# Performance work log

Measured on AMD Instinct MI355X. Metric: run time of the kernel, lower is better.

Reference implementation:

```python
import jax, jax.numpy as jnp
import numpy as np

N_CELLS_PER_SIDE = 16
MAX_K = 32
N_HEADS = 8
CHUNK = 128

_NEIGHBOR_OFFSETS = jnp.array([[-1, -1], [-1, 0], [-1, 1], [0, -1], [0, 0], [0, 1], [1, -1], [1, 0], [1, 1]], dtype=jnp.int32)


def cell_lookup(query_pos, cell_map, pos_min, pos_range):
    B, S, _ = query_pos.shape
    mpc = cell_map.shape[1]
    normalized = (query_pos - pos_min) / pos_range
    cell_xy = jnp.clip((normalized * N_CELLS_PER_SIDE).astype(jnp.int32), 0, N_CELLS_PER_SIDE - 1)
    nb = jnp.clip(cell_xy[:, :, None, :] + _NEIGHBOR_OFFSETS[None, None, :, :], 0, N_CELLS_PER_SIDE - 1)
    nidx = nb[..., 0] * N_CELLS_PER_SIDE + nb[..., 1]
    cand = cell_map[nidx].reshape(B, S, 9 * mpc)
    valid = cand >= 0
    return jnp.where(valid, cand, 0), valid


def threshold_gate(scores, tau, max_k):
    raw = scores - tau
    gate = jnp.where(raw > 0, raw, 1e-8 * jnp.exp(raw))
    eg = jnp.exp(gate) - 1.0
    k = min(max_k, scores.shape[-1])
    tv, _ = jax.lax.top_k(eg, k)
    eg = jnp.where(eg >= tv[:, :, -1:], eg, 0.0)
    gs = eg.sum(axis=-1, keepdims=True) + 1e-8
    strength = jnp.tanh(eg.max(axis=-1, keepdims=True))
    return eg / gs * strength


def setup_inputs() -> dict:
    key = jax.random.key(0)
    ks = jax.random.split(key, 16)
    B, S, D, N, P = 2, 1024, 512, 4096, 2
    n_cells, mpc = N_CELLS_PER_SIDE ** 2, 32
    return {
        "x": jax.random.normal(ks[0], (B, S, D), jnp.float32),
        "qk_pos": jax.random.uniform(ks[1], (B, S, P), jnp.float32),
        "v_pos": jax.random.uniform(ks[2], (B, S, P), jnp.float32),
        "tau_Q": jax.random.uniform(ks[3], (B, S, 1), jnp.float32),
        "tau_K": jax.random.uniform(ks[4], (B, S, 1), jnp.float32),
        "tau_V": jax.random.uniform(ks[5], (B, S, 1), jnp.float32),
        "qk_neurons": jax.random.normal(ks[6], (N, D), jnp.float32) / np.float32(np.sqrt(D)),
        "v_neurons": jax.random.normal(ks[7], (N, D), jnp.float32) / np.float32(np.sqrt(D)),
        "npos_qk": jax.random.uniform(ks[8], (N, P), jnp.float32),
        "npos_v": jax.random.uniform(ks[9], (N, P), jnp.float32),
        "cell_map_qk": jax.random.randint(ks[10], (n_cells, mpc), 0, N, jnp.int32),
        "cell_map_v": jax.random.randint(ks[11], (n_cells, mpc), 0, N, jnp.int32),
        "pos_min": jnp.zeros((P,), jnp.float32),
        "pos_range": jnp.ones((P,), jnp.float32),
        "expand_O": jax.random.normal(ks[12], (D, D), jnp.float32) * 0.02,
    }


def reference(x, qk_pos, v_pos, tau_Q, tau_K, tau_V, qk_neurons, v_neurons, npos_qk, npos_v, cell_map_qk, cell_map_v, pos_min, pos_range, expand_O):
    B, S, D = x.shape
    # full-sequence spatial cell lookup (small int tensors)
    ci_qk, m_qk = cell_lookup(qk_pos, cell_map_qk, pos_min, pos_range)
    ci_v, m_v = cell_lookup(v_pos, cell_map_v, pos_min, pos_range)
    ci_qk = jax.lax.stop_gradient(ci_qk)
    ci_v = jax.lax.stop_gradient(ci_v)
    nc = S // CHUNK  # S chosen divisible by CHUNK (no padding path needed)

    def chunks(a):
        return a.reshape(B, nc, CHUNK, *a.shape[2:]).swapaxes(0, 1)

    inp = tuple(map(chunks, (x, qk_pos, v_pos, tau_Q, tau_K, tau_V, ci_qk, m_qk, ci_v, m_v)))

    def step(carry, c):
        x_c, qkp, vp, tq, tk, tv, i_qk, mk, i_v, mv = c
        cand_qk = qk_neurons[i_qk]  # [B,C,n_cand,D]
        cand_v = v_neurons[i_v]
        act_qk = jnp.einsum('bsd,bsnd->bsn', x_c, cand_qk)
        act_v = jnp.einsum('bsd,bsnd->bsn', x_c, cand_v)
        s_qk = jnp.where(mk, act_qk, -1e9)
        s_v = jnp.where(mv, act_v, -1e9)
        gQ = threshold_gate(s_qk, tq, MAX_K)
        gK = threshold_gate(s_qk, tk, MAX_K)
        gV = threshold_gate(s_v, tv, MAX_K)
        Q_c = jnp.einsum('bsn,bsnd->bsd', act_qk * gQ * mk, cand_qk)
        K_c = jnp.einsum('bsn,bsnd->bsd', act_qk * gK * mk, cand_qk)
        V_c = jnp.einsum('bsn,bsnd->bsd', act_v * gV * mv, cand_v)
        pd_qk = jnp.sum((qkp[:, :, None, :] - npos_qk[i_qk]) ** 2, axis=-1)
        pl_qk = (jax.lax.stop_gradient(gQ) * pd_qk * mk).sum() / (mk.sum() + 1e-8)
        pd_v = jnp.sum((vp[:, :, None, :] - npos_v[i_v]) ** 2, axis=-1)
        pl_v = (jax.lax.stop_gradient(gV) * pd_v * mv).sum() / (mv.sum() + 1e-8)
        return carry, (Q_c, K_c, V_c, pl_qk + pl_v)

    _, (Qs, Ks, Vs, pls) = jax.lax.scan(step, 0, inp)

    def merge(a):
        return a.swapaxes(0, 1).reshape(B, S, D)

    Q, K, V = merge(Qs), merge(Ks), merge(Vs)
    pos_loss = pls.mean()  # == sum / n_chunks

    dh = D // N_HEADS
    Qh = Q.reshape(B, S, N_HEADS, dh).transpose(0, 2, 1, 3)
    Kh = K.reshape(B, S, N_HEADS, dh).transpose(0, 2, 1, 3)
    Vh = V.reshape(B, S, N_HEADS, dh).transpose(0, 2, 1, 3)
    scores = jnp.einsum('bhsd,bhtd->bhst', Qh, Kh) / jnp.sqrt(jnp.float32(dh))
    causal = jnp.tril(jnp.ones((S, S), dtype=jnp.bool_))
    scores = jnp.where(causal, scores, jnp.finfo(scores.dtype).min)
    attn = jax.nn.softmax(scores, axis=-1)
    out = jnp.einsum('bhst,bhtd->bhsd', attn, Vh)
    out = out.transpose(0, 2, 1, 3).reshape(B, S, D)
    out = out @ expand_O
    return out, pos_loss
```

## Files before the change

kernel.cpp:

```cpp
#include <hip/hip_runtime.h>
#include <math.h>

#define B_ 2
#define S_ 1024
#define D_ 512
#define N_ 4096
#define H_ 8
#define DH_ 64
#define NCAND 288
#define TOPK 32
#define NTOK (B_*S_)
#define NG2 1152

#define NROWS 16384
#define NSLOT_BH 8704
#define NSLOTS (16*NSLOT_BH)

typedef __attribute__((ext_vector_type(8))) short short8;
typedef __attribute__((ext_vector_type(4))) float f32x4;

__device__ __forceinline__ float wave_sum(float v) {
    #pragma unroll
    for (int o = 32; o; o >>= 1) v += __shfl_xor(v, o);
    return v;
}
__device__ __forceinline__ float wave_max(float v) {
    #pragma unroll
    for (int o = 32; o; o >>= 1) v = fmaxf(v, __shfl_xor(v, o));
    return v;
}
__device__ __forceinline__ ushort f2b_rn(float f) {
    unsigned u = __float_as_uint(f);
    return (ushort)((u + 0x7FFFu + ((u >> 16) & 1u)) >> 16);
}
__device__ __forceinline__ float b2f(ushort h) {
    return __uint_as_float(((unsigned)h) << 16);
}
__device__ __forceinline__ int swzi(int row, int c8) {
    return row * 64 + ((c8 ^ (row & 7)) << 3);
}

__global__ __launch_bounds__(1024) void sort_tokens_kernel(
    const float* __restrict__ qk_pos, const float* __restrict__ v_pos,
    const float* __restrict__ pos_min, const float* __restrict__ pos_range,
    int* __restrict__ order_qk, int* __restrict__ order_v,
    int2* __restrict__ desc_qk, int2* __restrict__ desc_v,
    float* __restrict__ posacc)
{
    __shared__ int hist[256], tmp[256], offs[256], startc[256], gcnt[256];
    const int t = threadIdx.x;
    const int pass = blockIdx.x;
    if (pass == 0 && t < 32) posacc[t] = 0.f;
    const float pm0 = pos_min[0], pm1 = pos_min[1];
    const float pr0 = pos_range[0], pr1 = pos_range[1];
    const float* pos = pass ? v_pos : qk_pos;
    int* order = pass ? order_v : order_qk;
    int2* desc = pass ? desc_v : desc_qk;
    if (t < NG2) desc[t] = make_int2(0, 0);
    if (t + 1024 < NG2) desc[t + 1024] = make_int2(0, 0);
    if (t < 256) hist[t] = 0;
    __syncthreads();
    int cell[2];
    #pragma unroll
    for (int k = 0; k < 2; k++) {
        int tok = t + k * 1024;
        float p0 = pos[tok * 2], p1 = pos[tok * 2 + 1];
        int cx = min(max((int)((p0 - pm0) / pr0 * 16.f), 0), 15);
        int cy = min(max((int)((p1 - pm1) / pr1 * 16.f), 0), 15);
        cell[k] = cx * 16 + cy;
        atomicAdd(&hist[cell[k]], 1);
    }
    __syncthreads();
    if (t < 256) tmp[t] = hist[t];
    __syncthreads();
    for (int d = 1; d < 256; d <<= 1) {
        int v = 0;
        if (t < 256 && t >= d) v = tmp[t - d];
        __syncthreads();
        if (t < 256) tmp[t] += v;
        __syncthreads();
    }
    if (t < 256) {
        startc[t] = tmp[t] - hist[t];
        offs[t]   = startc[t];
        gcnt[t]   = (hist[t] + 1) >> 1;
    }
    __syncthreads();
    #pragma unroll
    for (int k = 0; k < 2; k++) {
        int tok = t + k * 1024;
        int p = atomicAdd(&offs[cell[k]], 1);
        order[p] = tok;
    }
    __syncthreads();
    if (t < 256) tmp[t] = gcnt[t];
    __syncthreads();
    for (int d = 1; d < 256; d <<= 1) {
        int v = 0;
        if (t < 256 && t >= d) v = tmp[t - d];
        __syncthreads();
        if (t < 256) tmp[t] += v;
        __syncthreads();
    }
    if (t < 256) {
        int g0 = tmp[t] - gcnt[t];
        for (int k = 0; k < gcnt[t]; k++)
            desc[g0 + k] = make_int2(startc[t] + 2 * k, min(2, hist[t] - 2 * k));
    }
}

__global__ __launch_bounds__(256) void qkv_fused(
    const int2* __restrict__ desc_qk, const int* __restrict__ order_qk,
    const int2* __restrict__ desc_v,  const int* __restrict__ order_v,
    const float* __restrict__ x,
    const float* __restrict__ qk_pos, const float* __restrict__ v_pos,
    const float* __restrict__ tauQ, const float* __restrict__ tauK,
    const float* __restrict__ tauV,
    const float* __restrict__ qk_neurons, const float* __restrict__ v_neurons,
    const float* __restrict__ npos_qk, const float* __restrict__ npos_v,
    const int* __restrict__ cm_qk, const int* __restrict__ cm_v,
    const float* __restrict__ pos_min, const float* __restrict__ pos_range,
    float* __restrict__ Q, float* __restrict__ K, float* __restrict__ V,
    float* __restrict__ posacc)
{
    const int bid = blockIdx.x;
    const int role = bid & 1;
    const int g = bid >> 1;
    const int gid = (g & 7) * 144 + (g >> 3);
    const int2 dsc = role ? desc_v[gid] : desc_qk[gid];
    const int gstart = dsc.x, count = dsc.y;
    if (count == 0) return;

    const int*   order   = role ? order_v   : order_qk;
    const float* pose    = role ? v_pos     : qk_pos;
    const float* neurons = role ? v_neurons : qk_neurons;
    const float* npos    = role ? npos_v    : npos_qk;
    const int*   cmap    = role ? cm_v      : cm_qk;

    __shared__ int   idx[NCAND];
    __shared__ float msk[NCAND];
    __shared__ float act[2][NCAND];
    __shared__ int   ci[2][NCAND];
    __shared__ float cw1[2][NCAND], cw2[2][NCAND];
    __shared__ int   toks[2], cnt2[2];
    __shared__ float red[2][2][4];
    __shared__ float redc;

    const int t = threadIdx.x, wid = t >> 6, lane = t & 63;
    const int sub = lane & 15, grp = lane >> 4;
    if (t < 2) { toks[t] = order[gstart + min(t, count - 1)]; cnt2[t] = 0; }
    __syncthreads();
    const int token0 = toks[0];

    const float pm0 = pos_min[0], pm1 = pos_min[1];
    const float pr0 = pos_range[0], pr1 = pos_range[1];
    {
        const float p0 = pose[token0 * 2], p1 = pose[token0 * 2 + 1];
        const int cx = min(max((int)((p0 - pm0) / pr0 * 16.f), 0), 15);
        const int cy = min(max((int)((p1 - pm1) / pr1 * 16.f), 0), 15);
        for (int c = t; c < NCAND; c += 256) {
            int o = c >> 5, ms = c & 31;
            int nx = min(max(cx + o / 3 - 1, 0), 15), ny = min(max(cy + o % 3 - 1, 0), 15);
            int cand = cmap[(nx * 16 + ny) * 32 + ms];
            idx[c] = cand >= 0 ? cand : 0;
            msk[c] = cand >= 0 ? 1.f : 0.f;
        }
    }
    __syncthreads();

    float4 xr0[8], xr1[8];
    {
        const float4* xp0 = (const float4*)(x + (size_t)toks[0] * D_);
        const float4* xp1 = (const float4*)(x + (size_t)toks[1] * D_);
        #pragma unroll
        for (int k = 0; k < 8; k++) {
            xr0[k] = xp0[k * 16 + sub];
            xr1[k] = xp1[k * 16 + sub];
        }
    }

    const int cb = wid * 72;
    for (int u = 0; u < 72; u += 4) {
        const int c = cb + u + grp;
        const float4* rp = (const float4*)(neurons + (size_t)idx[c] * D_);
        float a0 = 0.f, a1 = 0.f, b0 = 0.f, b1 = 0.f;
        #pragma unroll
        for (int k = 0; k < 8; k += 2) {
            float4 r0 = rp[k * 16 + sub];
            float4 r1 = rp[(k + 1) * 16 + sub];
            a0 += xr0[k].x*r0.x + xr0[k].y*r0.y + xr0[k].z*r0.z + xr0[k].w*r0.w;
            a1 += xr1[k].x*r0.x + xr1[k].y*r0.y + xr1[k].z*r0.z + xr1[k].w*r0.w;
            b0 += xr0[k+1].x*r1.x + xr0[k+1].y*r1.y + xr0[k+1].z*r1.z + xr0[k+1].w*r1.w;
            b1 += xr1[k+1].x*r1.x + xr1[k+1].y*r1.y + xr1[k+1].z*r1.z + xr1[k+1].w*r1.w;
        }
        float f0 = a0 + b0, f1 = a1 + b1;
        #pragma unroll
        for (int o = 1; o <= 8; o <<= 1) {
            f0 += __shfl_xor(f0, o);
            f1 += __shfl_xor(f1, o);
        }
        if (sub == 0) {
            const float mv = msk[c];
            act[0][c] = (mv != 0.f) ? f0 : -1e9f;
            act[1][c] = (mv != 0.f) ? f1 : -1e9f;
        }
    }
    __syncthreads();

    const int tk = wid >> 1, sw = wid & 1, tt = t & 127;
    const int token = toks[tk];

    if (sw == 0) {
        unsigned ej[5];
        #pragma unroll
        for (int k = 0; k < 5; k++) {
            int j = lane + 64 * k;
            float f = (j < NCAND) ? act[tk][j] : -1e30f;
            unsigned uu = __float_as_uint(f);
            ej[k] = (uu & 0x80000000u) ? ~uu : (uu | 0x80000000u);
        }
        unsigned T = 0u;
        for (int bit = 31; bit >= 0; bit--) {
            const unsigned cand = T | (1u << bit);
            int c = 0;
            #pragma unroll
            for (int k = 0; k < 5; k++)
                c += __popcll(__ballot(ej[k] >= cand));
            if (c >= TOPK) T = cand;
        }
        int base = 0;
        const unsigned long long below = (lane == 0) ? 0ull
                                       : (~0ull >> (64 - lane));
        #pragma unroll
        for (int k = 0; k < 5; k++) {
            const unsigned long long mk2 = __ballot(ej[k] >= T);
            if (ej[k] >= T) {
                int pos = base + __popcll(mk2 & below);
                ci[tk][pos] = lane + 64 * k;
            }
            base += __popcll(mk2);
        }
        if (lane == 0) cnt2[tk] = base;
    }
    if (wid == 0) {
        float cmv = 0.f;
        for (int c = lane; c < NCAND; c += 64) cmv += msk[c];
        cmv = wave_sum(cmv);
        if (lane == 0) redc = cmv;
    }
    __syncthreads();
    const float cm = redc;
    const int n = cnt2[tk];

    if (role == 0) {
        const float tq = tauQ[token], tkk = tauK[token];
        float sQ = 0.f, sK = 0.f, mQ = 0.f, mK = 0.f;
        for (int p = tt; p < n; p += 128) {
            float s = act[tk][ci[tk][p]];
            float rq = s - tq;
            float gq = (rq > 0.f) ? rq : 1e-8f * __expf(rq);
            float egq = __expf(gq) - 1.f;
            float rk = s - tkk;
            float gk = (rk > 0.f) ? rk : 1e-8f * __expf(rk);
            float egk = __expf(gk) - 1.f;
            cw1[tk][p] = egq; cw2[tk][p] = egk;
            sQ += egq; sK += egk;
            mQ = fmaxf(mQ, egq); mK = fmaxf(mK, egk);
        }
        sQ = wave_sum(sQ); mQ = wave_max(mQ);
        sK = wave_sum(sK); mK = wave_max(mK);
        if (lane == 0) {
            red[tk][sw][0] = sQ; red[tk][sw][1] = mQ;
            red[tk][sw][2] = sK; red[tk][sw][3] = mK;
        }
        __syncthreads();
        const float scQ = tanhf(fmaxf(red[tk][0][1], red[tk][1][1]))
                        / (red[tk][0][0] + red[tk][1][0] + 1e-8f);
        const float scK = tanhf(fmaxf(red[tk][0][3], red[tk][1][3]))
                        / (red[tk][0][2] + red[tk][1][2] + 1e-8f);
        __syncthreads();

        const float qp0 = pose[token * 2], qp1 = pose[token * 2 + 1];
        float plq = 0.f;
        for (int p = tt; p < n; p += 128) {
            int e = ci[tk][p];
            int id = idx[e];
            float m = msk[e], a = act[tk][e];
            float gq = cw1[tk][p] * scQ;
            cw1[tk][p] = a * gq * m;
            cw2[tk][p] = a * cw2[tk][p] * scK * m;
            ci[tk][p] = id;
            float d0 = qp0 - npos[id * 2], d1 = qp1 - npos[id * 2 + 1];
            plq += gq * (d0 * d0 + d1 * d1) * m;
        }
        plq = wave_sum(plq);
        if (lane == 0) red[tk][sw][0] = plq;
        __syncthreads();
        if (tt == 0 && tk < count) {
            int chunk = (token & 1023) >> 7;
            atomicAdd(&posacc[chunk], red[tk][0][0] + red[tk][1][0]);
            atomicAdd(&posacc[8 + chunk], cm);
        }

        if (tk < count) {
            float4 qa = {0,0,0,0}, ka = {0,0,0,0};
            int p = 0;
            for (; p + 1 < n; p += 2) {
                const float4 rA = *(const float4*)(neurons + (size_t)ci[tk][p] * D_ + tt * 4);
                const float4 rB = *(const float4*)(neurons + (size_t)ci[tk][p + 1] * D_ + tt * 4);
                const float wA = cw1[tk][p], bA = cw2[tk][p];
                const float wB = cw1[tk][p + 1], bB = cw2[tk][p + 1];
                qa.x += wA * rA.x + wB * rB.x; qa.y += wA * rA.y + wB * rB.y;
                qa.z += wA * rA.z + wB * rB.z; qa.w += wA * rA.w + wB * rB.w;
                ka.x += bA * rA.x + bB * rB.x; ka.y += bA * rA.y + bB * rB.y;
                ka.z += bA * rA.z + bB * rB.z; ka.w += bA * rA.w + bB * rB.w;
            }
            if (p < n) {
                const float4 rA = *(const float4*)(neurons + (size_t)ci[tk][p] * D_ + tt * 4);
                const float wA = cw1[tk][p], bA = cw2[tk][p];
                qa.x += wA * rA.x; qa.y += wA * rA.y; qa.z += wA * rA.z; qa.w += wA * rA.w;
                ka.x += bA * rA.x; ka.y += bA * rA.y; ka.z += bA * rA.z; ka.w += bA * rA.w;
            }
            *(float4*)(Q + (size_t)token * D_ + tt * 4) = qa;
            *(float4*)(K + (size_t)token * D_ + tt * 4) = ka;
        }
    } else {
        const float tv = tauV[token];
        float sV = 0.f, mV = 0.f;
        for (int p = tt; p < n; p += 128) {
            float s = act[tk][ci[tk][p]];
            float rv = s - tv;
            float gv = (rv > 0.f) ? rv : 1e-8f * __expf(rv);
            float egv = __expf(gv) - 1.f;
            cw1[tk][p] = egv;
            sV += egv; mV = fmaxf(mV, egv);
        }
        sV = wave_sum(sV); mV = wave_max(mV);
        if (lane == 0) { red[tk][sw][0] = sV; red[tk][sw][1] = mV; }
        __syncthreads();
        const float scV = tanhf(fmaxf(red[tk][0][1], red[tk][1][1]))
                        / (red[tk][0][0] + red[tk][1][0] + 1e-8f);
        __syncthreads();

        const float vp0 = pose[token * 2], vp1 = pose[token * 2 + 1];
        float plv = 0.f;
        for (int p = tt; p < n; p += 128) {
            int e = ci[tk][p];
            int id = idx[e];
            float m = msk[e], a = act[tk][e];
            float gv = cw1[tk][p] * scV;
            cw1[tk][p] = a * gv * m;
            ci[tk][p] = id;
            float d0 = vp0 - npos[id * 2], d1 = vp1 - npos[id * 2 + 1];
            plv += gv * (d0 * d0 + d1 * d1) * m;
        }
        plv = wave_sum(plv);
        if (lane == 0) red[tk][sw][0] = plv;
        __syncthreads();
        if (tt == 0 && tk < count) {
            int chunk = (token & 1023) >> 7;
            atomicAdd(&posacc[16 + chunk], red[tk][0][0] + red[tk][1][0]);
            atomicAdd(&posacc[24 + chunk], cm);
        }

        if (tk < count) {
            float4 va = {0,0,0,0};
            int p = 0;
            for (; p + 1 < n; p += 2) {
                const float4 rA = *(const float4*)(neurons + (size_t)ci[tk][p] * D_ + tt * 4);
                const float4 rB = *(const float4*)(neurons + (size_t)ci[tk][p + 1] * D_ + tt * 4);
                const float wA = cw1[tk][p], wB = cw1[tk][p + 1];
                va.x += wA * rA.x + wB * rB.x; va.y += wA * rA.y + wB * rB.y;
                va.z += wA * rA.z + wB * rB.z; va.w += wA * rA.w + wB * rB.w;
            }
            if (p < n) {
                const float4 rA = *(const float4*)(neurons + (size_t)ci[tk][p] * D_ + tt * 4);
                const float wA = cw1[tk][p];
                va.x += wA * rA.x; va.y += wA * rA.y; va.z += wA * rA.z; va.w += wA * rA.w;
            }
            *(float4*)(V + (size_t)token * D_ + tt * 4) = va;
        }
    }
}

__global__ __launch_bounds__(256) void wprep_kernel(
    const float* __restrict__ W, ushort* __restrict__ Wth, ushort* __restrict__ Wtl)
{
    __shared__ float tile[64][65];
    const int bx = blockIdx.x & 7, by = blockIdx.x >> 3;
    const int t = threadIdx.x;
    const int r = t >> 4, c4 = (t & 15) * 4;
    #pragma unroll
    for (int rr = 0; rr < 64; rr += 16) {
        const float4 v = *(const float4*)(W + (size_t)(by * 64 + rr + r) * 512 + bx * 64 + c4);
        *(float4*)&tile[rr + r][c4] = v;
    }
    __syncthreads();
    #pragma unroll
    for (int cc = 0; cc < 64; cc += 16) {
        const int c = cc + r;
        ushort h[4], l[4];
        #pragma unroll
        for (int i = 0; i < 4; i++) {
            float f = tile[c4 + i][c];
            h[i] = f2b_rn(f);
            l[i] = f2b_rn(f - b2f(h[i]));
        }
        *(uint2*)&Wth[(size_t)(bx * 64 + c) * 512 + by * 64 + c4] = *(uint2*)h;
        *(uint2*)&Wtl[(size_t)(bx * 64 + c) * 512 + by * 64 + c4] = *(uint2*)l;
    }
}

__global__ __launch_bounds__(256, 2) void attn_partial_kernel(
    const float* __restrict__ Q, const float* __restrict__ K,
    const float* __restrict__ V,
    float* __restrict__ pm, float* __restrict__ pl, float* __restrict__ po)
{
    const int xx = blockIdx.x & 7;
    int kq = blockIdx.x >> 3;
    const int bh = xx + 8 * (kq >= 72);
    kq = (kq >= 72) ? kq - 72 : kq;
    int rblk = 0;
    while (kq >= 2 * (rblk + 1)) { kq -= 2 * (rblk + 1); rblk++; }
    const int sp = kq;
    const int b = bh >> 3, h = bh & 7;
    const int j0 = sp * 64;
    const int rbase = rblk * 128;

    __shared__ __align__(16) ushort sKhi[64 * 64], sKlo[64 * 64];
    __shared__ __align__(16) ushort sVthi[64 * 64], sVtlo[64 * 64];
    __shared__ __align__(16) float sPool[8192];

    const int t = threadIdx.x;
    const int w = t >> 6, lane = t & 63;
    const int g = lane >> 4, ln = lane & 15;

    {
        const int srow = t >> 2, scol = (t & 3) << 4;
        const float* Kg = K + ((size_t)(b * S_ + j0 + srow)) * D_ + h * DH_ + scol;
        const float* Vg = V + ((size_t)(b * S_ + j0 + srow)) * D_ + h * DH_ + scol;
        union { float4 f4[4]; float f[16]; } kf, vf;
        kf.f4[0] = *(const float4*)(Kg);
        kf.f4[1] = *(const float4*)(Kg + 4);
        kf.f4[2] = *(const float4*)(Kg + 8);
        kf.f4[3] = *(const float4*)(Kg + 12);
        vf.f4[0] = *(const float4*)(Vg);
        vf.f4[1] = *(const float4*)(Vg + 4);
        vf.f4[2] = *(const float4*)(Vg + 8);
        vf.f4[3] = *(const float4*)(Vg + 12);
        union { uint4 d[2]; ushort u[16]; } uh, ul;
        #pragma unroll
        for (int i = 0; i < 16; i++) {
            uh.u[i] = f2b_rn(kf.f[i]);
            ul.u[i] = f2b_rn(kf.f[i] - b2f(uh.u[i]));
        }
        const int c8 = (t & 3) << 1;
        *(uint4*)&sKhi[swzi(srow, c8)]     = uh.d[0];
        *(uint4*)&sKhi[swzi(srow, c8 + 1)] = uh.d[1];
        *(uint4*)&sKlo[swzi(srow, c8)]     = ul.d[0];
        *(uint4*)&sKlo[swzi(srow, c8 + 1)] = ul.d[1];
        #pragma unroll
        for (int i = 0; i < 16; i++) sPool[srow * 65 + scol + i] = vf.f[i];
    }
    __syncthreads();
    {
        const int drow = t >> 2, kcol = (t & 3) << 4;
        union { uint4 d[2]; ushort u[16]; } uh, ul;
        #pragma unroll
        for (int i = 0; i < 16; i++) {
            const float f = sPool[(kcol + i) * 65 + drow];
            uh.u[i] = f2b_rn(f);
            ul.u[i] = f2b_rn(f - b2f(uh.u[i]));
        }
        const int c8 = (t & 3) << 1;
        *(uint4*)&sVthi[swzi(drow, c8)]     = uh.d[0];
        *(uint4*)&sVthi[swzi(drow, c8 + 1)] = uh.d[1];
        *(uint4*)&sVtlo[swzi(drow, c8)]     = ul.d[0];
        *(uint4*)&sVtlo[swzi(drow, c8 + 1)] = ul.d[1];
    }
    __syncthreads();

    const int wrow = rbase + w * 32;
    if (wrow + 31 < j0) return;

    ushort* sPw = (ushort*)sPool + w * 4096;

    short8 qhi[2][2], qlo[2][2];
    #pragma unroll
    for (int qt = 0; qt < 2; qt++) {
        const int qrow = wrow + qt * 16 + ln;
        const float* Qg = Q + ((size_t)(b * S_ + qrow)) * D_ + h * DH_ + g * 8;
        #pragma unroll
        for (int ds = 0; ds < 2; ds++) {
            union { float4 f4[2]; float f[8]; } qf;
            qf.f4[0] = *(const float4*)(Qg + ds * 32);
            qf.f4[1] = *(const float4*)(Qg + ds * 32 + 4);
            union { short8 v; ushort u[8]; } uh, ul;
            #pragma unroll
            for (int i = 0; i < 8; i++) {
                uh.u[i] = f2b_rn(qf.f[i]);
                ul.u[i] = f2b_rn(qf.f[i] - b2f(uh.u[i]));
            }
            qhi[qt][ds] = uh.v; qlo[qt][ds] = ul.v;
        }
    }

    const f32x4 fzero = {0.f, 0.f, 0.f, 0.f};
    f32x4 sT[2][4];
    #pragma unroll
    for (int qt = 0; qt < 2; qt++)
        #pragma unroll
        for (int kt = 0; kt < 4; kt++)
            sT[qt][kt] = fzero;
    #pragma unroll
    for (int ds = 0; ds < 2; ds++) {
        #pragma unroll
        for (int kt = 0; kt < 4; kt++) {
            const int krow = kt * 16 + ln;
            const short8 khi = *(const short8*)&sKhi[swzi(krow, ds * 4 + g)];
            const short8 klo = *(const short8*)&sKlo[swzi(krow, ds * 4 + g)];
            #pragma unroll
            for (int qt = 0; qt < 2; qt++) {
                sT[qt][kt] = __builtin_amdgcn_mfma_f32_16x16x32_bf16(khi, qhi[qt][ds], sT[qt][kt], 0, 0, 0);
                sT[qt][kt] = __builtin_amdgcn_mfma_f32_16x16x32_bf16(khi, qlo[qt][ds], sT[qt][kt], 0, 0, 0);
                sT[qt][kt] = __builtin_amdgcn_mfma_f32_16x16x32_bf16(klo, qhi[qt][ds], sT[qt][kt], 0, 0, 0);
            }
        }
    }

    #pragma unroll
    for (int qt = 0; qt < 2; qt++) {
        const int qg = wrow + qt * 16 + ln;
        float pv[16];
        float mq = -1e30f;
        #pragma unroll
        for (int kt = 0; kt < 4; kt++)
            #pragma unroll
            for (int r = 0; r < 4; r++) {
                const int kg = j0 + kt * 16 + g * 4 + r;
                float s = sT[qt][kt][r] * 0.125f;
                s = (kg <= qg) ? s : -1e30f;
                pv[kt * 4 + r] = s;
                mq = fmaxf(mq, s);
            }
        mq = fmaxf(mq, __shfl_xor(mq, 16));
        mq = fmaxf(mq, __shfl_xor(mq, 32));
        const float base = (mq < -1e29f) ? 0.f : mq;
        float lq = 0.f;
        #pragma unroll
        for (int i = 0; i < 16; i++) {
            const float e = __expf(pv[i] - base);
            pv[i] = e;
            lq += e;
        }
        lq += __shfl_xor(lq, 16);
        lq += __shfl_xor(lq, 32);

        const int qrow = qt * 16 + ln;
        #pragma unroll
        for (int kt = 0; kt < 4; kt++) {
            union { uint2 d; ushort u[4]; } h4, l4;
            #pragma unroll
            for (int r = 0; r < 4; r++) {
                const float f = pv[kt * 4 + r];
                h4.u[r] = f2b_rn(f);
                l4.u[r] = f2b_rn(f - b2f(h4.u[r]));
            }
            const int c8 = kt * 2 + (g >> 1);
            const int idx = qrow * 64 + ((c8 ^ (qrow & 7)) << 3) + ((g & 1) << 2);
            *(uint2*)&sPw[idx] = h4.d;
            *(uint2*)&sPw[2048 + idx] = l4.d;
        }
        if (g == 0 && qg >= j0) {
            const int gr = qg >> 6;
            const size_t slot = (size_t)bh * NSLOT_BH + 32 * gr * (gr + 1)
                              + (size_t)(qg & 63) * (gr + 1) + sp;
            pm[slot] = mq; pl[slot] = lq;
        }
    }

    f32x4 ot[4][2];
    #pragma unroll
    for (int dt = 0; dt < 4; dt++)
        #pragma unroll
        for (int qt = 0; qt < 2; qt++)
            ot[dt][qt] = fzero;
    #pragma unroll
    for (int ks = 0; ks < 2; ks++) {
        short8 pfh[2], pfl[2];
        #pragma unroll
        for (int qt = 0; qt < 2; qt++) {
            const int qrow = qt * 16 + ln;
            const int idx = qrow * 64 + (((ks * 4 + g) ^ (qrow & 7)) << 3);
            pfh[qt] = *(const short8*)&sPw[idx];
            pfl[qt] = *(const short8*)&sPw[2048 + idx];
        }
        #pragma unroll
        for (int dt = 0; dt < 4; dt++) {
            const int drow = dt * 16 + ln;
            const short8 vh = *(const short8*)&sVthi[swzi(drow, ks * 4 + g)];
            const short8 vl = *(const short8*)&sVtlo[swzi(drow, ks * 4 + g)];
            #pragma unroll
            for (int qt = 0; qt < 2; qt++) {
                ot[dt][qt] = __builtin_amdgcn_mfma_f32_16x16x32_bf16(vh, pfh[qt], ot[dt][qt], 0, 0, 0);
                ot[dt][qt] = __builtin_amdgcn_mfma_f32_16x16x32_bf16(vh, pfl[qt], ot[dt][qt], 0, 0, 0);
                ot[dt][qt] = __builtin_amdgcn_mfma_f32_16x16x32_bf16(vl, pfh[qt], ot[dt][qt], 0, 0, 0);
            }
        }
    }

    #pragma unroll
    for (int qt = 0; qt < 2; qt++) {
        const int qg = wrow + qt * 16 + ln;
        if (qg < j0) continue;
        const int gr = qg >> 6;
        const size_t slot = (size_t)bh * NSLOT_BH + 32 * gr * (gr + 1)
                          + (size_t)(qg & 63) * (gr + 1) + sp;
        float* od = po + slot * 64 + g * 4;
        #pragma unroll
        for (int dt = 0; dt < 4; dt++)
            *(f32x4*)(od + dt * 16) = ot[dt][qt];
    }
}

__global__ __launch_bounds__(256) void attn_combine_kernel(
    const float* __restrict__ pm, const float* __restrict__ pl,
    const float* __restrict__ po, float* __restrict__ AO)
{
    const int gth = blockIdx.x * 256 + threadIdx.x;
    const int r = gth >> 6, d = gth & 63;
    const int i = r & 1023, bh = r >> 10;
    const int b = bh >> 3, h = bh & 7;
    const int g = i >> 6;
    const int ns = g + 1;
    const size_t slot0 = (size_t)bh * NSLOT_BH + 32 * g * (g + 1)
                       + (size_t)(i & 63) * (g + 1);
    float mstar = -INFINITY, lstar = 0.f, ostar = 0.f;
    for (int s = 0; s < ns; s++) {
        const float mi = pm[slot0 + s];
        const float nm = fmaxf(mstar, mi);
        const float a = __expf(mstar - nm);
        const float w = __expf(mi - nm);
        lstar = lstar * a + pl[slot0 + s] * w;
        ostar = ostar * a + po[(slot0 + s) * 64 + d] * w;
        mstar = nm;
    }
    AO[((size_t)(b * S_ + i)) * D_ + h * DH_ + d] = ostar / lstar;
}

__global__ __launch_bounds__(256) void proj_kernel(
    const float* __restrict__ A,
    const ushort* __restrict__ Wth, const ushort* __restrict__ Wtl,
    float* __restrict__ out)
{
    const int tb = (blockIdx.x >> 4) * 64;
    const int cb = (blockIdx.x & 15) * 32;
    const int t = threadIdx.x, w = t >> 6, lane = t & 63;
    const int ln = lane & 15, ko = (lane >> 4) * 8;
    const int tok = tb + w * 16 + ln;

    const f32x4 fz = {0.f, 0.f, 0.f, 0.f};
    f32x4 acc[2];
    acc[0] = fz; acc[1] = fz;

    const float* Ap = A + (size_t)tok * 512 + ko;
    #pragma unroll 4
    for (int ks = 0; ks < 512; ks += 32) {
        union { float4 f4[2]; float f[8]; } af;
        af.f4[0] = *(const float4*)(Ap + ks);
        af.f4[1] = *(const float4*)(Ap + ks + 4);
        union { short8 v; ushort u[8]; } ah, al;
        #pragma unroll
        for (int i = 0; i < 8; i++) {
            ah.u[i] = f2b_rn(af.f[i]);
            al.u[i] = f2b_rn(af.f[i] - b2f(ah.u[i]));
        }
        #pragma unroll
        for (int ct = 0; ct < 2; ct++) {
            const size_t wb = (size_t)(cb + ct * 16 + ln) * 512 + ks + ko;
            const short8 bh = *(const short8*)(Wth + wb);
            const short8 bl = *(const short8*)(Wtl + wb);
            acc[ct] = __builtin_amdgcn_mfma_f32_16x16x32_bf16(ah.v, bh, acc[ct], 0, 0, 0);
            acc[ct] = __builtin_amdgcn_mfma_f32_16x16x32_bf16(al.v, bh, acc[ct], 0, 0, 0);
            acc[ct] = __builtin_amdgcn_mfma_f32_16x16x32_bf16(ah.v, bl, acc[ct], 0, 0, 0);
        }
    }
    #pragma unroll
    for (int ct = 0; ct < 2; ct++) {
        #pragma unroll
        for (int r = 0; r < 4; r++) {
            const int row = tb + w * 16 + (lane >> 4) * 4 + r;
            out[(size_t)row * 512 + cb + ct * 16 + ln] = acc[ct][r];
        }
    }
}

__global__ void ploss_kernel(const float* __restrict__ acc, float* __restrict__ out) {
    float ssum = 0.f;
    for (int c = 0; c < 8; c++) {
        ssum += acc[c]      / (acc[8 + c]  + 1e-8f);
        ssum += acc[16 + c] / (acc[24 + c] + 1e-8f);
    }
    out[0] = ssum * 0.125f;
}

extern "C" void kernel_launch(void* const* d_in, const int* in_sizes, int n_in,
                              void* d_out, int out_size, void* d_ws, size_t ws_size,
                              hipStream_t stream) {
    const float* x          = (const float*)d_in[0];
    const float* qk_pos     = (const float*)d_in[1];
    const float* v_pos      = (const float*)d_in[2];
    const float* tauQ       = (const float*)d_in[3];
    const float* tauK       = (const float*)d_in[4];
    const float* tauV       = (const float*)d_in[5];
    const float* qk_neurons = (const float*)d_in[6];
    const float* v_neurons  = (const float*)d_in[7];
    const float* npos_qk    = (const float*)d_in[8];
    const float* npos_v     = (const float*)d_in[9];
    const int*   cm_qk      = (const int*)d_in[10];
    const int*   cm_v       = (const int*)d_in[11];
    const float* pos_min    = (const float*)d_in[12];
    const float* pos_range  = (const float*)d_in[13];
    const float* expand_O   = (const float*)d_in[14];

    float* ws = (float*)d_ws;
    const size_t TDf = (size_t)NTOK * D_;
    float* Q   = ws;
    float* K   = ws + TDf;
    float* V   = ws + 2 * TDf;
    float* AO  = ws + 3 * TDf;
    float* acc = ws + 4 * TDf;
    int*   order_qk = (int*)(ws + 4 * TDf + 64);
    int*   order_v  = order_qk + NTOK;
    int2*  desc_qk  = (int2*)(order_v + NTOK);
    int2*  desc_v   = desc_qk + NG2;
    const size_t head = 4 * TDf + 64 + 2 * NTOK + 4 * NG2;

    float* pm = ws + head;
    float* pl = pm + (size_t)NSLOTS;
    float* po = pl + (size_t)NSLOTS;
    ushort* Wth = (ushort*)(po + (size_t)NSLOTS * 64);
    ushort* Wtl = Wth + 512 * 512;

    float* out = (float*)d_out;

    sort_tokens_kernel<<<2, 1024, 0, stream>>>(qk_pos, v_pos, pos_min, pos_range,
                                               order_qk, order_v, desc_qk, desc_v,
                                               acc);
    wprep_kernel<<<64, 256, 0, stream>>>(expand_O, Wth, Wtl);
    qkv_fused<<<2 * NG2, 256, 0, stream>>>(desc_qk, order_qk, desc_v, order_v,
                                           x, qk_pos, v_pos, tauQ, tauK, tauV,
                                           qk_neurons, v_neurons, npos_qk, npos_v,
                                           cm_qk, cm_v, pos_min, pos_range,
                                           Q, K, V, acc);
    attn_partial_kernel<<<1152, 256, 0, stream>>>(Q, K, V, pm, pl, po);
    attn_combine_kernel<<<(NROWS * 64) / 256, 256, 0, stream>>>(pm, pl, po, AO);
    proj_kernel<<<512, 256, 0, stream>>>(AO, Wth, Wtl, out);
    ploss_kernel<<<1, 1, 0, stream>>>(acc, out + TDf);
}
```

Baseline: 256.0 us.

## Emit bf16 hi/lo Q and K from QKV kernel, read directly in attention

The QKV kernel now writes Q and K as split bf16 hi/lo pairs, so the attention kernel no longer repeats the fp32-to-bf16 split on every tile it loads. K is read straight from global memory into MFMA operands instead of going through shared memory, which drops the K LDS buffers and their staging. The single-thread ploss kernel is folded into the projection kernel to save a launch. The trade-off is that K loads are now scattered global reads served from cache rather than swizzled LDS reads. Q and K traffic stays the same size, since two 16-bit halves replace one 32-bit value.

```diff
diff --git a/kernel.cpp b/kernel.cpp
--- a/kernel.cpp
+++ b/kernel.cpp
@@ -120,7 +120,9 @@
     const float* __restrict__ npos_qk, const float* __restrict__ npos_v,
     const int* __restrict__ cm_qk, const int* __restrict__ cm_v,
     const float* __restrict__ pos_min, const float* __restrict__ pos_range,
-    float* __restrict__ Q, float* __restrict__ K, float* __restrict__ V,
+    ushort* __restrict__ Qh, ushort* __restrict__ Ql,
+    ushort* __restrict__ Kh, ushort* __restrict__ Kl,
+    float* __restrict__ V,
     float* __restrict__ posacc)
 {
     const int bid = blockIdx.x;
@@ -321,8 +323,19 @@
                 qa.x += wA * rA.x; qa.y += wA * rA.y; qa.z += wA * rA.z; qa.w += wA * rA.w;
                 ka.x += bA * rA.x; ka.y += bA * rA.y; ka.z += bA * rA.z; ka.w += bA * rA.w;
             }
-            *(float4*)(Q + (size_t)token * D_ + tt * 4) = qa;
-            *(float4*)(K + (size_t)token * D_ + tt * 4) = ka;
+            float qv[4] = {qa.x, qa.y, qa.z, qa.w};
+            float kv[4] = {ka.x, ka.y, ka.z, ka.w};
+            ushort qh4[4], ql4[4], kh4[4], kl4[4];
+            #pragma unroll
+            for (int i = 0; i < 4; i++) {
+                qh4[i] = f2b_rn(qv[i]); ql4[i] = f2b_rn(qv[i] - b2f(qh4[i]));
+                kh4[i] = f2b_rn(kv[i]); kl4[i] = f2b_rn(kv[i] - b2f(kh4[i]));
+            }
+            const size_t qo = (size_t)token * D_ + tt * 4;
+            *(uint2*)(Qh + qo) = *(uint2*)qh4;
+            *(uint2*)(Ql + qo) = *(uint2*)ql4;
+            *(uint2*)(Kh + qo) = *(uint2*)kh4;
+            *(uint2*)(Kl + qo) = *(uint2*)kl4;
         }
     } else {
         const float tv = tauV[token];
@@ -412,7 +425,8 @@
 }
 
 __global__ __launch_bounds__(256, 2) void attn_partial_kernel(
-    const float* __restrict__ Q, const float* __restrict__ K,
+    const ushort* __restrict__ Qh, const ushort* __restrict__ Ql,
+    const ushort* __restrict__ Kh, const ushort* __restrict__ Kl,
     const float* __restrict__ V,
     float* __restrict__ pm, float* __restrict__ pl, float* __restrict__ po)
 {
@@ -427,7 +441,6 @@
     const int j0 = sp * 64;
     const int rbase = rblk * 128;
 
-    __shared__ __align__(16) ushort sKhi[64 * 64], sKlo[64 * 64];
     __shared__ __align__(16) ushort sVthi[64 * 64], sVtlo[64 * 64];
     __shared__ __align__(16) float sPool[8192];
 
@@ -437,30 +450,15 @@
 
     {
         const int srow = t >> 2, scol = (t & 3) << 4;
-        const float* Kg = K + ((size_t)(b * S_ + j0 + srow)) * D_ + h * DH_ + scol;
         const float* Vg = V + ((size_t)(b * S_ + j0 + srow)) * D_ + h * DH_ + scol;
-        union { float4 f4[4]; float f[16]; } kf, vf;
-        kf.f4[0] = *(const float4*)(Kg);
-        kf.f4[1] = *(const float4*)(Kg + 4);
-        kf.f4[2] = *(const float4*)(Kg + 8);
-        kf.f4[3] = *(const float4*)(Kg + 12);
-        vf.f4[0] = *(const float4*)(Vg);
-        vf.f4[1] = *(const float4*)(Vg + 4);
-        vf.f4[2] = *(const float4*)(Vg + 8);
-        vf.f4[3] = *(const float4*)(Vg + 12);
-        union { uint4 d[2]; ushort u[16]; } uh, ul;
-        #pragma unroll
-        for (int i = 0; i < 16; i++) {
-            uh.u[i] = f2b_rn(kf.f[i]);
-            ul.u[i] = f2b_rn(kf.f[i] - b2f(uh.u[i]));
-        }
-        const int c8 = (t & 3) << 1;
-        *(uint4*)&sKhi[swzi(srow, c8)]     = uh.d[0];
-        *(uint4*)&sKhi[swzi(srow, c8 + 1)] = uh.d[1];
-        *(uint4*)&sKlo[swzi(srow, c8)]     = ul.d[0];
-        *(uint4*)&sKlo[swzi(srow, c8 + 1)] = ul.d[1];
-        #pragma unroll
-        for (int i = 0; i < 16; i++) sPool[srow * 65 + scol + i] = vf.f[i];
+        float4 v0 = *(const float4*)(Vg);
+        float4 v1 = *(const float4*)(Vg + 4);
+        float4 v2 = *(const float4*)(Vg + 8);
+        float4 v3 = *(const float4*)(Vg + 12);
+        *(float4*)&sPool[srow * 65 + scol]      = v0;
+        *(float4*)&sPool[srow * 65 + scol + 4]  = v1;
+        *(float4*)&sPool[srow * 65 + scol + 8]  = v2;
+        *(float4*)&sPool[srow * 65 + scol + 12] = v3;
     }
     __syncthreads();
     {
@@ -489,19 +487,11 @@
     #pragma unroll
     for (int qt = 0; qt < 2; qt++) {
         const int qrow = wrow + qt * 16 + ln;
-        const float* Qg = Q + ((size_t)(b * S_ + qrow)) * D_ + h * DH_ + g * 8;
+        const size_t qb = ((size_t)(b * S_ + qrow)) * D_ + h * DH_ + g * 8;
         #pragma unroll
         for (int ds = 0; ds < 2; ds++) {
-            union { float4 f4[2]; float f[8]; } qf;
-            qf.f4[0] = *(const float4*)(Qg + ds * 32);
-            qf.f4[1] = *(const float4*)(Qg + ds * 32 + 4);
-            union { short8 v; ushort u[8]; } uh, ul;
-            #pragma unroll
-            for (int i = 0; i < 8; i++) {
-                uh.u[i] = f2b_rn(qf.f[i]);
-                ul.u[i] = f2b_rn(qf.f[i] - b2f(uh.u[i]));
-            }
-            qhi[qt][ds] = uh.v; qlo[qt][ds] = ul.v;
+            qhi[qt][ds] = *(const short8*)(Qh + qb + ds * 32);
+            qlo[qt][ds] = *(const short8*)(Ql + qb + ds * 32);
         }
     }
 
@@ -517,8 +507,9 @@
         #pragma unroll
         for (int kt = 0; kt < 4; kt++) {
             const int krow = kt * 16 + ln;
-            const short8 khi = *(const short8*)&sKhi[swzi(krow, ds * 4 + g)];
-            const short8 klo = *(const short8*)&sKlo[swzi(krow, ds * 4 + g)];
+            const size_t kb = ((size_t)(b * S_ + j0 + krow)) * D_ + h * DH_ + ds * 32 + g * 8;
+            const short8 khi = *(const short8*)(Kh + kb);
+            const short8 klo = *(const short8*)(Kl + kb);
             #pragma unroll
             for (int qt = 0; qt < 2; qt++) {
                 sT[qt][kt] = __builtin_amdgcn_mfma_f32_16x16x32_bf16(khi, qhi[qt][ds], sT[qt][kt], 0, 0, 0);
@@ -651,8 +642,17 @@
 __global__ __launch_bounds__(256) void proj_kernel(
     const float* __restrict__ A,
     const ushort* __restrict__ Wth, const ushort* __restrict__ Wtl,
-    float* __restrict__ out)
+    const float* __restrict__ acc,
+    float* __restrict__ out, float* __restrict__ outp)
 {
+    if (blockIdx.x == 0 && threadIdx.x == 0) {
+        float ssum = 0.f;
+        for (int c = 0; c < 8; c++) {
+            ssum += acc[c]      / (acc[8 + c]  + 1e-8f);
+            ssum += acc[16 + c] / (acc[24 + c] + 1e-8f);
+        }
+        outp[0] = ssum * 0.125f;
+    }
     const int tb = (blockIdx.x >> 4) * 64;
     const int cb = (blockIdx.x & 15) * 32;
     const int t = threadIdx.x, w = t >> 6, lane = t & 63;
@@ -660,8 +660,8 @@
     const int tok = tb + w * 16 + ln;
 
     const f32x4 fz = {0.f, 0.f, 0.f, 0.f};
-    f32x4 acc[2];
-    acc[0] = fz; acc[1] = fz;
+    f32x4 acc2[2];
+    acc2[0] = fz; acc2[1] = fz;
 
     const float* Ap = A + (size_t)tok * 512 + ko;
     #pragma unroll 4
@@ -680,9 +680,9 @@
             const size_t wb = (size_t)(cb + ct * 16 + ln) * 512 + ks + ko;
             const short8 bh = *(const short8*)(Wth + wb);
             const short8 bl = *(const short8*)(Wtl + wb);
-            acc[ct] = __builtin_amdgcn_mfma_f32_16x16x32_bf16(ah.v, bh, acc[ct], 0, 0, 0);
-            acc[ct] = __builtin_amdgcn_mfma_f32_16x16x32_bf16(al.v, bh, acc[ct], 0, 0, 0);
-            acc[ct] = __builtin_amdgcn_mfma_f32_16x16x32_bf16(ah.v, bl, acc[ct], 0, 0, 0);
+            acc2[ct] = __builtin_amdgcn_mfma_f32_16x16x32_bf16(ah.v, bh, acc2[ct], 0, 0, 0);
+            acc2[ct] = __builtin_amdgcn_mfma_f32_16x16x32_bf16(al.v, bh, acc2[ct], 0, 0, 0);
+            acc2[ct] = __builtin_amdgcn_mfma_f32_16x16x32_bf16(ah.v, bl, acc2[ct], 0, 0, 0);
         }
     }
     #pragma unroll
@@ -690,18 +690,9 @@
         #pragma unroll
         for (int r = 0; r < 4; r++) {
             const int row = tb + w * 16 + (lane >> 4) * 4 + r;
-            out[(size_t)row * 512 + cb + ct * 16 + ln] = acc[ct][r];
-        }
-    }
-}
-
-__global__ void ploss_kernel(const float* __restrict__ acc, float* __restrict__ out) {
-    float ssum = 0.f;
-    for (int c = 0; c < 8; c++) {
-        ssum += acc[c]      / (acc[8 + c]  + 1e-8f);
-        ssum += acc[16 + c] / (acc[24 + c] + 1e-8f);
-    }
-    out[0] = ssum * 0.125f;
+            out[(size_t)row * 512 + cb + ct * 16 + ln] = acc2[ct][r];
+        }
+    }
 }
 
 extern "C" void kernel_launch(void* const* d_in, const int* in_sizes, int n_in,
@@ -725,8 +716,8 @@
 
     float* ws = (float*)d_ws;
     const size_t TDf = (size_t)NTOK * D_;
-    float* Q   = ws;
-    float* K   = ws + TDf;
+    float* Qf  = ws;
+    float* Kf  = ws + TDf;
     float* V   = ws + 2 * TDf;
     float* AO  = ws + 3 * TDf;
     float* acc = ws + 4 * TDf;
@@ -742,6 +733,11 @@
     ushort* Wth = (ushort*)(po + (size_t)NSLOTS * 64);
     ushort* Wtl = Wth + 512 * 512;
 
+    ushort* Qh = (ushort*)Qf;
+    ushort* Ql = Qh + TDf;
+    ushort* Kh = (ushort*)Kf;
+    ushort* Kl = Kh + TDf;
+
     float* out = (float*)d_out;
 
     sort_tokens_kernel<<<2, 1024, 0, stream>>>(qk_pos, v_pos, pos_min, pos_range,
@@ -752,9 +748,8 @@
                                            x, qk_pos, v_pos, tauQ, tauK, tauV,
                                            qk_neurons, v_neurons, npos_qk, npos_v,
                                            cm_qk, cm_v, pos_min, pos_range,
-                                           Q, K, V, acc);
-    attn_partial_kernel<<<1152, 256, 0, stream>>>(Q, K, V, pm, pl, po);
+                                           Qh, Ql, Kh, Kl, V, acc);
+    attn_partial_kernel<<<1152, 256, 0, stream>>>(Qh, Ql, Kh, Kl, V, pm, pl, po);
     attn_combine_kernel<<<(NROWS * 64) / 256, 256, 0, stream>>>(pm, pl, po, AO);
-    proj_kernel<<<512, 256, 0, stream>>>(AO, Wth, Wtl, out);
-    ploss_kernel<<<1, 1, 0, stream>>>(acc, out + TDf);
-}
+    proj_kernel<<<512, 256, 0, stream>>>(AO, Wth, Wtl, acc, out, out + TDf);
+}
```

New measurement: 283.8 us. 10.8% more time.
